# Performance work log

Measured on AMD Instinct MI355X. Metric: run time of the kernel, lower is better.

Reference implementation:

```python
import jax, jax.numpy as jnp
import numpy as np

N_NODES = 50000
N_EDGES = 800000
IN_DIM = 128
HID_DIM = 64
OUT_DIM = 40
N_REL = 8


def setup_inputs() -> dict:
    key = jax.random.key(0)
    ks = jax.random.split(key, 12)
    x = jax.random.normal(ks[0], (N_NODES, IN_DIM), dtype=jnp.float32)
    edge_index = jax.random.randint(ks[1], (2, N_EDGES), 0, N_NODES, dtype=jnp.int64)
    edge_type = jax.random.randint(ks[2], (N_EDGES,), 0, N_REL, dtype=jnp.int64)
    s = 0.05
    W1 = jax.random.normal(ks[3], (N_REL, IN_DIM, HID_DIM), dtype=jnp.float32) * s
    root1 = jax.random.normal(ks[4], (IN_DIM, HID_DIM), dtype=jnp.float32) * s
    b1 = jnp.zeros((HID_DIM,), dtype=jnp.float32)
    W2 = jax.random.normal(ks[5], (N_REL, HID_DIM, HID_DIM), dtype=jnp.float32) * s
    root2 = jax.random.normal(ks[6], (HID_DIM, HID_DIM), dtype=jnp.float32) * s
    b2 = jnp.zeros((HID_DIM,), dtype=jnp.float32)
    Wl = jax.random.normal(ks[7], (HID_DIM, OUT_DIM), dtype=jnp.float32) * s
    bl = jnp.zeros((OUT_DIM,), dtype=jnp.float32)
    return {"x": x, "edge_index": edge_index, "edge_type": edge_type,
            "W1": W1, "root1": root1, "b1": b1,
            "W2": W2, "root2": root2, "b2": b2,
            "Wl": Wl, "bl": bl}


def _rgcn_conv(x, W, Wroot, b, src, dst, edge_type):
    # PyG RGCNConv (no bases/blocks, aggr='mean'):
    #   out[i] = sum_r mean_{(j->i) of rel r} (x[j] @ W[r]) + x[i] @ Wroot + b
    N = x.shape[0]
    R = W.shape[0]
    h = jnp.einsum('ni,rio->rno', x, W)        # [R, N, out]
    msgs = h[edge_type, src]                   # [E, out] edge gather
    seg = edge_type * N + dst                  # per (relation, dst) segment
    sums = jax.ops.segment_sum(msgs, seg, num_segments=R * N)
    cnt = jax.ops.segment_sum(jnp.ones((msgs.shape[0],), x.dtype), seg,
                              num_segments=R * N)
    mean = sums / jnp.maximum(cnt, 1.0)[:, None]
    agg = mean.reshape(R, N, -1).sum(axis=0)   # sum over relations
    return agg + x @ Wroot + b


def reference(x, edge_index, edge_type, W1, root1, b1, W2, root2, b2, Wl, bl):
    src, dst = edge_index[0], edge_index[1]
    h = jax.nn.relu(_rgcn_conv(x, W1, root1, b1, src, dst, edge_type))
    # dropout is identity in eval mode
    h = jax.nn.relu(_rgcn_conv(h, W2, root2, b2, src, dst, edge_type))
    logits = h @ Wl + bl
    return jax.nn.log_softmax(logits, axis=1)
```

## Files before the change

kernel.cpp:

```cpp
#include <hip/hip_runtime.h>
#include <hip/hip_bf16.h>
#include <cmath>


#define IN_DIM 128
#define HID 64
#define OUT_DIM 40
#define NREL 8
#define NCOLS 576
#define CAP 64
#define CSTR 16

typedef __attribute__((ext_vector_type(8))) short short8;
typedef __attribute__((ext_vector_type(4))) short short4v;
typedef __attribute__((ext_vector_type(4))) float floatx4;
typedef __attribute__((ext_vector_type(2))) float f32x2;

static __device__ __forceinline__ short f2bf(float f) {
  __hip_bfloat16 h = __float2bfloat16(f);
  return __builtin_bit_cast(short, h);
}
static __device__ __forceinline__ float bflo(unsigned int u) {
  return __int_as_float(u << 16);
}
static __device__ __forceinline__ float bfhi(unsigned int u) {
  return __int_as_float(u & 0xffff0000u);
}
static __device__ __forceinline__ unsigned int packbf(float x, float y) {
  unsigned int lo = (unsigned short)f2bf(x);
  unsigned int hi = (unsigned short)f2bf(y);
  return lo | (hi << 16);
}

__global__ void pack_bt(const float* __restrict__ W1, const float* __restrict__ root1,
                        short* __restrict__ Bt1,
                        const float* __restrict__ W2, const float* __restrict__ root2,
                        short* __restrict__ Bt2,
                        int* __restrict__ cursor, int nzero4) {
  const int PB1 = (NCOLS * IN_DIM + 255) / 256;
  const int PB2 = (NCOLS * HID + 255) / 256;
  int b = blockIdx.x;
  if (b < PB1) {
    int i = b * 256 + threadIdx.x;
    if (i >= NCOLS * IN_DIM) return;
    int c = i / IN_DIM, k = i % IN_DIM;
    float v = (c < NREL * HID)
      ? W1[((size_t)(c >> 6) * IN_DIM + k) * HID + (c & 63)]
      : root1[(size_t)k * HID + (c - NREL * HID)];
    Bt1[i] = f2bf(v);
  } else if (b < PB1 + PB2) {
    int i = (b - PB1) * 256 + threadIdx.x;
    if (i >= NCOLS * HID) return;
    int c = i / HID, k = i % HID;
    float v = (c < NREL * HID)
      ? W2[((size_t)(c >> 6) * HID + k) * HID + (c & 63)]
      : root2[(size_t)k * HID + (c - NREL * HID)];
    Bt2[i] = f2bf(v);
  } else {
    int i = (b - PB1 - PB2) * 256 + threadIdx.x;
    if (i < nzero4) {
      int4 z; z.x = 0; z.y = 0; z.z = 0; z.w = 0;
      ((int4*)cursor)[i] = z;
    }
  }
}

__global__ __launch_bounds__(256) void scatter_ev(
    const int* __restrict__ src, const int* __restrict__ dst,
    const int* __restrict__ et,
    int* __restrict__ cursor, int* __restrict__ ev, int E)
{
  int e = blockIdx.x * 256 + threadIdx.x;
  if (e >= E) return;
  int d = dst[e];
  int pos = atomicAdd(&cursor[d * CSTR], 1);
  if (pos < CAP)
    __builtin_nontemporal_store((src[e] << 3) | et[e], &ev[d * CAP + pos]);
}

template<int K, int AMODE>
__device__ __forceinline__ void gemm_dev(
    short* As, short* Bs,
    const void* __restrict__ Aptr, const short* __restrict__ Bt,
    const float* __restrict__ bias, short* __restrict__ H,
    unsigned short* __restrict__ AGG, int M, int row0)
{
  constexpr int AST = K + 8;
  constexpr int CB = K / 8;
  constexpr int NCH = 64 * CB / 256;
  int tid = threadIdx.x;
  int wv = tid >> 6, lane = tid & 63;
  int lm = lane & 15, quad = lane >> 4;

  int bn[NCH], bko[NCH];
  #pragma unroll
  for (int j = 0; j < NCH; ++j) {
    int i = tid + j * 256;
    bn[j] = i / CB; bko[j] = i % CB;
  }

  short8 breg[NCH];
  #pragma unroll
  for (int j = 0; j < NCH; ++j)
    breg[j] = *(const short8*)(Bt + (unsigned)(bn[j] * K + bko[j] * 8));

  if (AMODE == 0) {
    const float* A = (const float*)Aptr;
    constexpr int CH = K / 4;
    for (int i = tid; i < 64 * CH; i += 256) {
      int r = i / CH, kq = i % CH;
      int gr = row0 + r; if (gr >= M) gr = M - 1;
      float4 v = *(const float4*)(A + (unsigned)(gr * K + kq * 4));
      short4v s;
      s.x = f2bf(v.x); s.y = f2bf(v.y); s.z = f2bf(v.z); s.w = f2bf(v.w);
      *(short4v*)(As + r * AST + kq * 4) = s;
    }
  } else {
    const short* A = (const short*)Aptr;
    constexpr int CH = K / 8;
    for (int i = tid; i < 64 * CH; i += 256) {
      int r = i / CH, ko = i % CH;
      int gr = row0 + r; if (gr >= M) gr = M - 1;
      short8 v = *(const short8*)(A + (unsigned)(gr * K + ko * 8));
      #pragma unroll
      for (int j = 0; j < 8; ++j)
        if ((unsigned short)v[j] & 0x8000u) v[j] = 0;
      *(short8*)(As + r * AST + ko * 8) = v;
    }
  }

  const short* ap = As + (16 * wv + lm) * AST + quad * 8;
  int rowg = row0 + 16 * wv + lm;

  for (int cy = 0; cy < 9; ++cy) {
    #pragma unroll
    for (int j = 0; j < NCH; ++j)
      *(short8*)(Bs + bn[j] * AST + bko[j] * 8) = breg[j];
    __syncthreads();

    if (cy < 8) {
      #pragma unroll
      for (int j = 0; j < NCH; ++j)
        breg[j] = *(const short8*)(
            Bt + (unsigned)(((cy + 1) * 64 + bn[j]) * K + bko[j] * 8));
    }

    floatx4 acc[4] = {{0,0,0,0},{0,0,0,0},{0,0,0,0},{0,0,0,0}};
    #pragma unroll
    for (int ks = 0; ks < K / 32; ++ks) {
      short8 a = *(const short8*)(ap + ks * 32);
      #pragma unroll
      for (int nb = 0; nb < 4; ++nb) {
        short8 b = *(const short8*)(Bs + (nb * 16 + lm) * AST + ks * 32 + quad * 8);
        acc[nb] = __builtin_amdgcn_mfma_f32_16x16x32_bf16(b, a, acc[nb], 0, 0, 0);
      }
    }
    __syncthreads();

    if (cy < 8) {
      if (rowg < M) {
        short* hrow = H + (unsigned)rowg * (NREL * HID) + cy * 64 + quad * 4;
        #pragma unroll
        for (int nb = 0; nb < 4; ++nb) {
          short4v s;
          s.x = f2bf(acc[nb][0]); s.y = f2bf(acc[nb][1]);
          s.z = f2bf(acc[nb][2]); s.w = f2bf(acc[nb][3]);
          *(short4v*)(hrow + nb * 16) = s;
        }
      }
    } else {
      if (rowg < M) {
        unsigned short* arow = AGG + (unsigned)rowg * HID + quad * 4;
        #pragma unroll
        for (int nb = 0; nb < 4; ++nb) {
          float4 bv = *(const float4*)(bias + nb * 16 + quad * 4);
          short4v s;
          s.x = f2bf(acc[nb][0] + bv.x); s.y = f2bf(acc[nb][1] + bv.y);
          s.z = f2bf(acc[nb][2] + bv.z); s.w = f2bf(acc[nb][3] + bv.w);
          *(short4v*)(arow + nb * 16) = s;
        }
      }
    }
  }
}

__global__ __launch_bounds__(256, 4) void gemm1_mfma(
    const float* __restrict__ A, const short* __restrict__ Bt,
    const float* __restrict__ bias, short* __restrict__ H,
    unsigned short* __restrict__ AGG, int M)
{
  constexpr int AST = IN_DIM + 8;
  __shared__ short As[64 * AST];
  __shared__ short Bs[64 * AST];
  gemm_dev<IN_DIM, 0>(As, Bs, A, Bt, bias, H, AGG, M, blockIdx.x * 64);
}

__global__ __launch_bounds__(256, 4) void gemm2_mfma(
    const unsigned short* __restrict__ A, const short* __restrict__ Bt,
    const float* __restrict__ bias, short* __restrict__ H,
    unsigned short* __restrict__ AGG, int M)
{
  constexpr int AST = HID + 8;
  __shared__ short As[64 * AST];
  __shared__ short Bs[64 * AST];
  gemm_dev<HID, 1>(As, Bs, A, Bt, bias, H, AGG, M, blockIdx.x * 64);
}

static __device__ __forceinline__ void agg_half2(
    const uint2* __restrict__ Hu2, const int* __restrict__ evrow,
    int cnt, int qloc, int sub, float wreg, int h,
    float& a0, float& a1, float& a2, float& a3)
{
  int npass = (cnt + 15) >> 4;
  f32x2 A01 = {a0, a1}, A23 = {a2, a3};
  for (int P = 0; P < npass; ++P) {
    const int4* pp = (const int4*)(evrow + P * 16 + qloc * 8);
    int4 v0 = pp[0], v1 = pp[1];
    int vv[8] = {v0.x, v0.y, v0.z, v0.w, v1.x, v1.y, v1.z, v1.w};
    int sb = P * 16 + qloc * 8;
    uint2 hv[8];
    float ww[8];
    #pragma unroll
    for (int i = 0; i < 8; ++i) {
      bool ok = (sb + i) < cnt;
      int v = ok ? vv[i] : 0;
      hv[i] = Hu2[(unsigned)v * 16u + (unsigned)sub];
      float w = __shfl(wreg, h * 32 + (v & 7), 64);
      ww[i] = ok ? w : 0.f;
    }
    #pragma unroll
    for (int i = 0; i < 8; ++i) {
      f32x2 w2 = {ww[i], ww[i]};
      f32x2 h01 = {bflo(hv[i].x), bfhi(hv[i].x)};
      f32x2 h23 = {bflo(hv[i].y), bfhi(hv[i].y)};
      A01 += h01 * w2;
      A23 += h23 * w2;
    }
  }
  a0 = A01.x; a1 = A01.y; a2 = A23.x; a3 = A23.y;
  a0 += __shfl_xor(a0, 16, 64);
  a1 += __shfl_xor(a1, 16, 64);
  a2 += __shfl_xor(a2, 16, 64);
  a3 += __shfl_xor(a3, 16, 64);
}

static __device__ __forceinline__ float rel_weight(
    const int* __restrict__ evr, int cnt, int lhl, int h)
{
  int e0 = evr[lhl], e1 = evr[lhl + 32];
  bool v0 = lhl < cnt, v1 = (lhl + 32) < cnt;
  int r0 = e0 & 7, r1 = e1 & 7;
  unsigned long long hm = 0xffffffffull << (h * 32);
  int myrel = lhl & 7;
  int c = 0;
  #pragma unroll
  for (int r = 0; r < 8; ++r) {
    unsigned long long m0 = __ballot(v0 && (r0 == r));
    unsigned long long m1 = __ballot(v1 && (r1 == r));
    int cr = __popcll(m0 & hm) + __popcll(m1 & hm);
    if (myrel == r) c = cr;
  }
  return (c > 0) ? (1.0f / (float)c) : 0.0f;
}

__global__ __launch_bounds__(256) void csr_agg(
    const short* __restrict__ H, const int* __restrict__ cursor,
    const int* __restrict__ ev, unsigned short* __restrict__ AGG, int N)
{
  int tid = threadIdx.x;
  int wv = tid >> 6, lane = tid & 63;
  int h = lane >> 5, lhl = lane & 31, qloc = lhl >> 4, sub = lhl & 15;
  int d = blockIdx.x * 8 + wv * 2 + h;
  int dc = d < N ? d : N - 1;

  int cnt = cursor[dc * CSTR]; if (cnt > CAP) cnt = CAP;
  const int* evr = ev + dc * CAP;
  float wreg = rel_weight(evr, cnt, lhl, h);

  float a0 = 0.f, a1 = 0.f, a2 = 0.f, a3 = 0.f;
  uint2* aggrow = (uint2*)(AGG + (size_t)dc * HID);
  if (qloc == 0) {
    uint2 iv = aggrow[sub];
    a0 = bflo(iv.x); a1 = bfhi(iv.x); a2 = bflo(iv.y); a3 = bfhi(iv.y);
  }
  agg_half2((const uint2*)H, evr, cnt, qloc, sub, wreg, h, a0, a1, a2, a3);
  if (d < N && qloc == 0) {
    uint2 ov;
    ov.x = packbf(a0, a1);
    ov.y = packbf(a2, a3);
    aggrow[sub] = ov;
  }
}

__global__ __launch_bounds__(256) void csr_agg_final(
    const short* __restrict__ H, const int* __restrict__ cursor,
    const int* __restrict__ ev, const unsigned short* __restrict__ AGG,
    const float* __restrict__ Wl, const float* __restrict__ bl,
    float* __restrict__ out, int N)
{
  __shared__ float sWl[HID * OUT_DIM];
  __shared__ float sbl[OUT_DIM];
  __shared__ float sh[8][HID];
  int tid = threadIdx.x;
  int wv = tid >> 6, lane = tid & 63;
  int h = lane >> 5, lhl = lane & 31, qloc = lhl >> 4, sub = lhl & 15;
  int d = blockIdx.x * 8 + wv * 2 + h;
  int dc = d < N ? d : N - 1;

  int cnt = cursor[dc * CSTR]; if (cnt > CAP) cnt = CAP;
  uint2 iv = ((const uint2*)(AGG + (size_t)dc * HID))[sub];
  const int* evr = ev + dc * CAP;
  float wreg = rel_weight(evr, cnt, lhl, h);

  for (int i = tid; i < HID * OUT_DIM; i += 256) sWl[i] = Wl[i];
  if (tid < OUT_DIM) sbl[tid] = bl[tid];
  __syncthreads();

  float a0 = 0.f, a1 = 0.f, a2 = 0.f, a3 = 0.f;
  if (qloc == 0) {
    a0 = bflo(iv.x); a1 = bfhi(iv.x); a2 = bflo(iv.y); a3 = bfhi(iv.y);
  }
  agg_half2((const uint2*)H, evr, cnt, qloc, sub, wreg, h, a0, a1, a2, a3);
  if (qloc == 0) {
    float4 v;
    v.x = fmaxf(a0, 0.f); v.y = fmaxf(a1, 0.f);
    v.z = fmaxf(a2, 0.f); v.w = fmaxf(a3, 0.f);
    *(float4*)(&sh[wv * 2 + h][4 * sub]) = v;
  }
  __syncthreads();

  #pragma unroll
  for (int ii = 0; ii < 2; ++ii) {
    int dd = blockIdx.x * 8 + wv * 2 + ii;
    const float* row = sh[wv * 2 + ii];
    float logit = -__builtin_inff();
    if (lane < OUT_DIM) {
      float t = sbl[lane];
      #pragma unroll 8
      for (int k = 0; k < HID; ++k) t += row[k] * sWl[k * OUT_DIM + lane];
      logit = t;
    }
    float m = logit;
    #pragma unroll
    for (int o = 32; o > 0; o >>= 1) m = fmaxf(m, __shfl_xor(m, o, 64));
    float ex = (lane < OUT_DIM) ? expf(logit - m) : 0.f;
    float s = ex;
    #pragma unroll
    for (int o = 32; o > 0; o >>= 1) s += __shfl_xor(s, o, 64);
    if (dd < N && lane < OUT_DIM)
      out[(size_t)dd * OUT_DIM + lane] = logit - m - logf(s);
  }
}

extern "C" void kernel_launch(void* const* d_in, const int* in_sizes, int n_in,
                              void* d_out, int out_size, void* d_ws, size_t ws_size,
                              hipStream_t stream) {
  const float* x     = (const float*)d_in[0];
  const int*   eidx  = (const int*)d_in[1];
  const int*   etype = (const int*)d_in[2];
  const float* W1    = (const float*)d_in[3];
  const float* root1 = (const float*)d_in[4];
  const float* b1    = (const float*)d_in[5];
  const float* W2    = (const float*)d_in[6];
  const float* root2 = (const float*)d_in[7];
  const float* b2    = (const float*)d_in[8];
  const float* Wl    = (const float*)d_in[9];
  const float* bl    = (const float*)d_in[10];

  int N = in_sizes[0] / IN_DIM;
  int E = in_sizes[2];
  const int* srcp = eidx;
  const int* dstp = eidx + E;

  char* ws = (char*)d_ws;
  size_t off = 0;
  auto alloc = [&](size_t bytes) -> char* {
    char* p = ws + off;
    off += (bytes + 255) & ~(size_t)255;
    return p;
  };
  short* Bt1    = (short*)alloc((size_t)NCOLS * IN_DIM * 2);
  short* Bt2    = (short*)alloc((size_t)NCOLS * HID * 2);
  int*   cursor = (int*)alloc((size_t)N * CSTR * 4);
  int*   ev     = (int*)alloc((size_t)N * CAP * 4);
  short* H1     = (short*)alloc((size_t)N * NREL * HID * 2);
  short* H2     = (short*)alloc((size_t)N * NREL * HID * 2);
  unsigned short* AGG1 = (unsigned short*)alloc((size_t)N * HID * 2);
  unsigned short* AGG2 = (unsigned short*)alloc((size_t)N * HID * 2);

  const int PB1 = (NCOLS * IN_DIM + 255) / 256;
  const int PB2 = (NCOLS * HID + 255) / 256;
  int nzero4 = (N * CSTR) / 4;
  int ZB = (nzero4 + 255) / 256;
  pack_bt<<<PB1 + PB2 + ZB, 256, 0, stream>>>(W1, root1, Bt1, W2, root2, Bt2,
                                              cursor, nzero4);

  int GB = (N + 63) / 64;
  int SB = (E + 255) / 256;
  scatter_ev<<<SB, 256, 0, stream>>>(srcp, dstp, etype, cursor, ev, E);

  gemm1_mfma<<<GB, 256, 0, stream>>>(x, Bt1, b1, H1, AGG1, N);

  csr_agg<<<(N + 7) / 8, 256, 0, stream>>>(H1, cursor, ev, AGG1, N);

  gemm2_mfma<<<GB, 256, 0, stream>>>(AGG1, Bt2, b2, H2, AGG2, N);

  csr_agg_final<<<(N + 7) / 8, 256, 0, stream>>>(H2, cursor, ev, AGG2,
                                                 Wl, bl, (float*)d_out, N);
}
```

Baseline: 258.8 us.

## Fuse edge scatter into GEMM1 launch and restructure CSR aggregation loads

Merges the scatter_ev kernel into the first GEMM kernel as extra blocks, so the edge bucketing and the layer-1 transform run in one launch and can overlap. The aggregation kernels now load the first 32 edge entries up front as vectors and compute per-relation counts from those registers, falling back to ballots only for the entries past 32. The neighbor-row loads are issued before the count math, and the Wl shared-memory staging moves after aggregation. This aims to cut launch overhead and hide gather latency, at the cost of more registers and the scatter blocks sharing the GEMM's shared-memory footprint.

```diff
diff --git a/kernel.cpp b/kernel.cpp
--- a/kernel.cpp
+++ b/kernel.cpp
@@ -65,19 +65,6 @@
   }
 }
 
-__global__ __launch_bounds__(256) void scatter_ev(
-    const int* __restrict__ src, const int* __restrict__ dst,
-    const int* __restrict__ et,
-    int* __restrict__ cursor, int* __restrict__ ev, int E)
-{
-  int e = blockIdx.x * 256 + threadIdx.x;
-  if (e >= E) return;
-  int d = dst[e];
-  int pos = atomicAdd(&cursor[d * CSTR], 1);
-  if (pos < CAP)
-    __builtin_nontemporal_store((src[e] << 3) | et[e], &ev[d * CAP + pos]);
-}
-
 template<int K, int AMODE>
 __device__ __forceinline__ void gemm_dev(
     short* As, short* Bs,
@@ -184,15 +171,27 @@
   }
 }
 
-__global__ __launch_bounds__(256, 4) void gemm1_mfma(
+__global__ __launch_bounds__(256, 4) void gemm1_scatter(
     const float* __restrict__ A, const short* __restrict__ Bt,
     const float* __restrict__ bias, short* __restrict__ H,
-    unsigned short* __restrict__ AGG, int M)
+    unsigned short* __restrict__ AGG, int M, int SB,
+    const int* __restrict__ src, const int* __restrict__ dst,
+    const int* __restrict__ et,
+    int* __restrict__ cursor, int* __restrict__ ev, int E)
 {
   constexpr int AST = IN_DIM + 8;
   __shared__ short As[64 * AST];
   __shared__ short Bs[64 * AST];
-  gemm_dev<IN_DIM, 0>(As, Bs, A, Bt, bias, H, AGG, M, blockIdx.x * 64);
+  if ((int)blockIdx.x >= SB) {
+    gemm_dev<IN_DIM, 0>(As, Bs, A, Bt, bias, H, AGG, M, (blockIdx.x - SB) * 64);
+  } else {
+    int e = blockIdx.x * 256 + threadIdx.x;
+    if (e >= E) return;
+    int d = dst[e];
+    int pos = atomicAdd(&cursor[d * CSTR], 1);
+    if (pos < CAP)
+      __builtin_nontemporal_store((src[e] << 3) | et[e], &ev[d * CAP + pos]);
+  }
 }
 
 __global__ __launch_bounds__(256, 4) void gemm2_mfma(
@@ -206,35 +205,104 @@
   gemm_dev<HID, 1>(As, Bs, A, Bt, bias, H, AGG, M, blockIdx.x * 64);
 }
 
-static __device__ __forceinline__ void agg_half2(
-    const uint2* __restrict__ Hu2, const int* __restrict__ evrow,
-    int cnt, int qloc, int sub, float wreg, int h,
+static __device__ __forceinline__ void agg_dst(
+    const uint2* __restrict__ Hu2, const int* __restrict__ evr,
+    int4 e0, int4 e1, int4 e2, int4 e3,
+    int cnt, int qloc, int sub, int lhl, int h,
     float& a0, float& a1, float& a2, float& a3)
 {
-  int npass = (cnt + 15) >> 4;
+  int vv0[8] = {e0.x, e0.y, e0.z, e0.w, e1.x, e1.y, e1.z, e1.w};
+  int vv1[8] = {e2.x, e2.y, e2.z, e2.w, e3.x, e3.y, e3.z, e3.w};
+  int base0 = qloc * 8, base1 = 16 + qloc * 8;
+  uint2 hv[8];
+
+  #pragma unroll
+  for (int i = 0; i < 8; ++i) {
+    bool ok = (base0 + i) < cnt;
+    int v = ok ? vv0[i] : 0;
+    hv[i] = Hu2[(unsigned)v * 16u + (unsigned)sub];
+  }
+
+  int myrel = lhl & 7;
+  int c = 0;
+  #pragma unroll
+  for (int i = 0; i < 8; ++i)
+    c += ((base0 + i) < cnt && (vv0[i] & 7) == myrel) ? 1 : 0;
+  #pragma unroll
+  for (int i = 0; i < 8; ++i)
+    c += ((base1 + i) < cnt && (vv1[i] & 7) == myrel) ? 1 : 0;
+  c += __shfl_xor(c, 16, 64);
+  if (cnt > 32) {
+    int eu = evr[32 + lhl];
+    bool valid = (32 + lhl) < cnt;
+    unsigned long long hm = 0xffffffffull << (h * 32);
+    int rr = eu & 7;
+    #pragma unroll
+    for (int r = 0; r < 8; ++r) {
+      unsigned long long m = __ballot(valid && rr == r);
+      int cr = __popcll(m & hm);
+      if (myrel == r) c += cr;
+    }
+  }
+  float wreg = (c > 0) ? (1.0f / (float)c) : 0.0f;
+
   f32x2 A01 = {a0, a1}, A23 = {a2, a3};
-  for (int P = 0; P < npass; ++P) {
-    const int4* pp = (const int4*)(evrow + P * 16 + qloc * 8);
-    int4 v0 = pp[0], v1 = pp[1];
-    int vv[8] = {v0.x, v0.y, v0.z, v0.w, v1.x, v1.y, v1.z, v1.w};
-    int sb = P * 16 + qloc * 8;
-    uint2 hv[8];
-    float ww[8];
+  #pragma unroll
+  for (int i = 0; i < 8; ++i) {
+    bool ok = (base0 + i) < cnt;
+    float w0 = __shfl(wreg, h * 32 + (vv0[i] & 7), 64);
+    float w = ok ? w0 : 0.f;
+    f32x2 w2 = {w, w};
+    f32x2 h01 = {bflo(hv[i].x), bfhi(hv[i].x)};
+    f32x2 h23 = {bflo(hv[i].y), bfhi(hv[i].y)};
+    A01 += h01 * w2;
+    A23 += h23 * w2;
+  }
+  if (cnt > 16) {
     #pragma unroll
     for (int i = 0; i < 8; ++i) {
-      bool ok = (sb + i) < cnt;
-      int v = ok ? vv[i] : 0;
+      bool ok = (base1 + i) < cnt;
+      int v = ok ? vv1[i] : 0;
       hv[i] = Hu2[(unsigned)v * 16u + (unsigned)sub];
-      float w = __shfl(wreg, h * 32 + (v & 7), 64);
-      ww[i] = ok ? w : 0.f;
     }
     #pragma unroll
     for (int i = 0; i < 8; ++i) {
-      f32x2 w2 = {ww[i], ww[i]};
+      bool ok = (base1 + i) < cnt;
+      float w0 = __shfl(wreg, h * 32 + (vv1[i] & 7), 64);
+      float w = ok ? w0 : 0.f;
+      f32x2 w2 = {w, w};
       f32x2 h01 = {bflo(hv[i].x), bfhi(hv[i].x)};
       f32x2 h23 = {bflo(hv[i].y), bfhi(hv[i].y)};
       A01 += h01 * w2;
       A23 += h23 * w2;
+    }
+  }
+  if (cnt > 32) {
+    #pragma unroll
+    for (int P = 2; P < 4; ++P) {
+      if (cnt > P * 16) {
+        const int4* pp = (const int4*)(evr + P * 16 + qloc * 8);
+        int4 f0 = pp[0], f1 = pp[1];
+        int vv[8] = {f0.x, f0.y, f0.z, f0.w, f1.x, f1.y, f1.z, f1.w};
+        int bs = P * 16 + qloc * 8;
+        #pragma unroll
+        for (int i = 0; i < 8; ++i) {
+          bool ok = (bs + i) < cnt;
+          int v = ok ? vv[i] : 0;
+          hv[i] = Hu2[(unsigned)v * 16u + (unsigned)sub];
+        }
+        #pragma unroll
+        for (int i = 0; i < 8; ++i) {
+          bool ok = (bs + i) < cnt;
+          float w0 = __shfl(wreg, h * 32 + (vv[i] & 7), 64);
+          float w = ok ? w0 : 0.f;
+          f32x2 w2 = {w, w};
+          f32x2 h01 = {bflo(hv[i].x), bfhi(hv[i].x)};
+          f32x2 h23 = {bflo(hv[i].y), bfhi(hv[i].y)};
+          A01 += h01 * w2;
+          A23 += h23 * w2;
+        }
+      }
     }
   }
   a0 = A01.x; a1 = A01.y; a2 = A23.x; a3 = A23.y;
@@ -244,25 +312,6 @@
   a3 += __shfl_xor(a3, 16, 64);
 }
 
-static __device__ __forceinline__ float rel_weight(
-    const int* __restrict__ evr, int cnt, int lhl, int h)
-{
-  int e0 = evr[lhl], e1 = evr[lhl + 32];
-  bool v0 = lhl < cnt, v1 = (lhl + 32) < cnt;
-  int r0 = e0 & 7, r1 = e1 & 7;
-  unsigned long long hm = 0xffffffffull << (h * 32);
-  int myrel = lhl & 7;
-  int c = 0;
-  #pragma unroll
-  for (int r = 0; r < 8; ++r) {
-    unsigned long long m0 = __ballot(v0 && (r0 == r));
-    unsigned long long m1 = __ballot(v1 && (r1 == r));
-    int cr = __popcll(m0 & hm) + __popcll(m1 & hm);
-    if (myrel == r) c = cr;
-  }
-  return (c > 0) ? (1.0f / (float)c) : 0.0f;
-}
-
 __global__ __launch_bounds__(256) void csr_agg(
     const short* __restrict__ H, const int* __restrict__ cursor,
     const int* __restrict__ ev, unsigned short* __restrict__ AGG, int N)
@@ -273,17 +322,23 @@
   int d = blockIdx.x * 8 + wv * 2 + h;
   int dc = d < N ? d : N - 1;
 
-  int cnt = cursor[dc * CSTR]; if (cnt > CAP) cnt = CAP;
+  int cnt = cursor[dc * CSTR];
   const int* evr = ev + dc * CAP;
-  float wreg = rel_weight(evr, cnt, lhl, h);
+  const int4* p0 = (const int4*)(evr + qloc * 8);
+  int4 e0 = p0[0], e1 = p0[1];
+  const int4* p1 = (const int4*)(evr + 16 + qloc * 8);
+  int4 e2 = p1[0], e3 = p1[1];
+  uint2* aggrow = (uint2*)(AGG + (size_t)dc * HID);
+  uint2 iv = {0, 0};
+  if (qloc == 0) iv = aggrow[sub];
+  if (cnt > CAP) cnt = CAP;
 
   float a0 = 0.f, a1 = 0.f, a2 = 0.f, a3 = 0.f;
-  uint2* aggrow = (uint2*)(AGG + (size_t)dc * HID);
   if (qloc == 0) {
-    uint2 iv = aggrow[sub];
     a0 = bflo(iv.x); a1 = bfhi(iv.x); a2 = bflo(iv.y); a3 = bfhi(iv.y);
   }
-  agg_half2((const uint2*)H, evr, cnt, qloc, sub, wreg, h, a0, a1, a2, a3);
+  agg_dst((const uint2*)H, evr, e0, e1, e2, e3, cnt, qloc, sub, lhl, h,
+          a0, a1, a2, a3);
   if (d < N && qloc == 0) {
     uint2 ov;
     ov.x = packbf(a0, a1);
@@ -307,26 +362,30 @@
   int d = blockIdx.x * 8 + wv * 2 + h;
   int dc = d < N ? d : N - 1;
 
-  int cnt = cursor[dc * CSTR]; if (cnt > CAP) cnt = CAP;
+  int cnt = cursor[dc * CSTR];
+  const int* evr = ev + dc * CAP;
+  const int4* p0 = (const int4*)(evr + qloc * 8);
+  int4 e0 = p0[0], e1 = p0[1];
+  const int4* p1 = (const int4*)(evr + 16 + qloc * 8);
+  int4 e2 = p1[0], e3 = p1[1];
   uint2 iv = ((const uint2*)(AGG + (size_t)dc * HID))[sub];
-  const int* evr = ev + dc * CAP;
-  float wreg = rel_weight(evr, cnt, lhl, h);
-
-  for (int i = tid; i < HID * OUT_DIM; i += 256) sWl[i] = Wl[i];
-  if (tid < OUT_DIM) sbl[tid] = bl[tid];
-  __syncthreads();
+  if (cnt > CAP) cnt = CAP;
 
   float a0 = 0.f, a1 = 0.f, a2 = 0.f, a3 = 0.f;
   if (qloc == 0) {
     a0 = bflo(iv.x); a1 = bfhi(iv.x); a2 = bflo(iv.y); a3 = bfhi(iv.y);
   }
-  agg_half2((const uint2*)H, evr, cnt, qloc, sub, wreg, h, a0, a1, a2, a3);
+  agg_dst((const uint2*)H, evr, e0, e1, e2, e3, cnt, qloc, sub, lhl, h,
+          a0, a1, a2, a3);
   if (qloc == 0) {
     float4 v;
     v.x = fmaxf(a0, 0.f); v.y = fmaxf(a1, 0.f);
     v.z = fmaxf(a2, 0.f); v.w = fmaxf(a3, 0.f);
     *(float4*)(&sh[wv * 2 + h][4 * sub]) = v;
   }
+
+  for (int i = tid; i < HID * OUT_DIM; i += 256) sWl[i] = Wl[i];
+  if (tid < OUT_DIM) sbl[tid] = bl[tid];
   __syncthreads();
 
   #pragma unroll
@@ -397,9 +456,8 @@
 
   int GB = (N + 63) / 64;
   int SB = (E + 255) / 256;
-  scatter_ev<<<SB, 256, 0, stream>>>(srcp, dstp, etype, cursor, ev, E);
-
-  gemm1_mfma<<<GB, 256, 0, stream>>>(x, Bt1, b1, H1, AGG1, N);
+  gemm1_scatter<<<SB + GB, 256, 0, stream>>>(x, Bt1, b1, H1, AGG1, N, SB,
+                                             srcp, dstp, etype, cursor, ev, E);
 
   csr_agg<<<(N + 7) / 8, 256, 0, stream>>>(H1, cursor, ev, AGG1, N);
 
```

Result: slower. 266.4 us (+2.9%).
